# Kernel tuning notes

Measured on AMD Instinct MI355X. Metric: run time of the kernel, lower is better.

The kernel has to match this reference:

```python
import jax, jax.numpy as jnp
import numpy as np

D = 6
EPS = 1e-5


def layer_norm(x, w, b):
    m = jnp.mean(x, axis=-1, keepdims=True)
    v = jnp.mean(jnp.square(x - m), axis=-1, keepdims=True)
    return (x - m) * jax.lax.rsqrt(v + EPS) * w + b


def setup_inputs() -> dict:
    key = jax.random.key(0)
    ks = jax.random.split(key, 8)
    B, S = 8192, 128
    scale = 0.2
    return {
        "x": jax.random.normal(ks[0], (B, S, D), jnp.float32),
        "ln1_w": jnp.ones((D,), jnp.float32),
        "ln1_b": jnp.zeros((D,), jnp.float32),
        "wqkv": jax.random.normal(ks[1], (D, 3 * D), jnp.float32) * scale,
        "bqkv": jnp.zeros((3 * D,), jnp.float32),
        "wo": jax.random.normal(ks[2], (D, D), jnp.float32) * scale,
        "bo": jnp.zeros((D,), jnp.float32),
        "ln2_w": jnp.ones((D,), jnp.float32),
        "ln2_b": jnp.zeros((D,), jnp.float32),
        "w1": jax.random.normal(ks[3], (D, D), jnp.float32) * scale,
        "b1": jnp.zeros((D,), jnp.float32),
        "w2": jax.random.normal(ks[4], (D, D), jnp.float32) * scale,
        "b2": jnp.zeros((D,), jnp.float32),
    }


def reference(x, ln1_w, ln1_b, wqkv, bqkv, wo, bo, ln2_w, ln2_b, w1, b1, w2, b2):
    B, S, _ = x.shape
    # --- attention sub-block: x = x + attn(ln1(x)) ---
    h = layer_norm(x, ln1_w, ln1_b)                      # [B,S,D]
    qkv = h @ wqkv + bqkv                                # [B,S,3D]
    q, k, v = jnp.split(qkv, 3, axis=-1)
    scores = jnp.einsum('bqd,bkd->bqk', q, k) / jnp.sqrt(jnp.asarray(D, x.dtype))
    causal = jnp.tril(jnp.ones((S, S), bool))            # [S,S]
    scores = jnp.where(causal, scores, jnp.asarray(-1e9, x.dtype))
    attn = jax.nn.softmax(scores, axis=-1)               # [B,S,S]
    o = jnp.einsum('bqk,bkd->bqd', attn, v) @ wo + bo
    x = x + o
    # --- FFN sub-block: x = x + W2 @ gelu(W1 @ ln2(x)) ---
    h2 = layer_norm(x, ln2_w, ln2_b)
    ff = jax.nn.gelu(h2 @ w1 + b1, approximate=False) @ w2 + b2
    return x + ff
```

## Files before the change

### kernel.cpp

```cpp
#include <hip/hip_runtime.h>
#include <cmath>


typedef float v2f  __attribute__((ext_vector_type(2)));
typedef short s8v  __attribute__((ext_vector_type(8)));
typedef float f16v __attribute__((ext_vector_type(16)));

constexpr int D = 6;
constexpr int S = 128;
#define EPS 1e-5f
#define RSQRT_D 0.4082482904638631f
#define LOG2E   1.4426950408889634f

#define EXP2F(x) __builtin_amdgcn_exp2f(x)
#define RCPF(x)  __builtin_amdgcn_rcpf(x)

union U4 { uint32_t u[4]; s8v v; };

__device__ __forceinline__ uint32_t pkbf(float hi, float lo) {
    return __builtin_amdgcn_perm(__builtin_bit_cast(uint32_t, hi),
                                 __builtin_bit_cast(uint32_t, lo),
                                 0x07060302u);
}
__device__ __forceinline__ uint16_t bf16t(float x) {
    return (uint16_t)(__builtin_bit_cast(uint32_t, x) >> 16);
}

__global__ __launch_bounds__(S, 3) void txblock_kernel(
    const float* __restrict__ x,
    const float* __restrict__ ln1_w, const float* __restrict__ ln1_b,
    const float* __restrict__ wqkv,  const float* __restrict__ bqkv,
    const float* __restrict__ wo,    const float* __restrict__ bo,
    const float* __restrict__ ln2_w, const float* __restrict__ ln2_b,
    const float* __restrict__ w1,    const float* __restrict__ b1,
    const float* __restrict__ w2,    const float* __restrict__ b2,
    float* __restrict__ out)
{
    __shared__ uint32_t qlds[S][8];
    __shared__ uint32_t klds[S][8];
    __shared__ uint16_t vt[8][S];
    __shared__ float    obuf[S][8];

    const int b = blockIdx.x;
    const int s = threadIdx.x;
    const float* xrow = x + ((size_t)b * S + s) * D;
    float*      orow = out + ((size_t)b * S + s) * D;

    v2f xv01 = ((const v2f*)xrow)[0];
    v2f xv23 = ((const v2f*)xrow)[1];
    v2f xv45 = ((const v2f*)xrow)[2];
    float xv[D] = {xv01[0], xv01[1], xv23[0], xv23[1], xv45[0], xv45[1]};

    float m = 0.f;
    #pragma unroll
    for (int d = 0; d < D; ++d) m += xv[d];
    m *= (1.0f / D);
    float var = 0.f;
    #pragma unroll
    for (int d = 0; d < D; ++d) { float t = xv[d] - m; var += t * t; }
    var *= (1.0f / D);
    float rstd = rsqrtf(var + EPS);
    float h1[D];
    #pragma unroll
    for (int d = 0; d < D; ++d)
        h1[d] = (xv[d] - m) * rstd * ln1_w[d] + ln1_b[d];

    float q[D], kk[D], vv[D];
    #pragma unroll
    for (int j = 0; j < D; ++j) {
        float aq = bqkv[j], ak = bqkv[D + j], av = bqkv[2 * D + j];
        #pragma unroll
        for (int d = 0; d < D; ++d) {
            const float* wrow = wqkv + d * 3 * D;
            aq += h1[d] * wrow[j];
            ak += h1[d] * wrow[D + j];
            av += h1[d] * wrow[2 * D + j];
        }
        q[j]  = aq * (RSQRT_D * LOG2E);
        kk[j] = ak;
        vv[j] = av;
    }

    qlds[s][0] = pkbf(q[1], q[0]);
    qlds[s][1] = pkbf(q[3], q[2]);
    qlds[s][2] = pkbf(q[5], q[4]);
    qlds[s][3] = 0; qlds[s][4] = 0; qlds[s][5] = 0; qlds[s][6] = 0; qlds[s][7] = 0;
    klds[s][0] = pkbf(kk[1], kk[0]);
    klds[s][1] = pkbf(kk[3], kk[2]);
    klds[s][2] = pkbf(kk[5], kk[4]);
    klds[s][3] = 0; klds[s][4] = 0; klds[s][5] = 0; klds[s][6] = 0; klds[s][7] = 0;
    #pragma unroll
    for (int d = 0; d < D; ++d) vt[d][s] = bf16t(vv[d]);
    vt[6][s] = 0x3F80;
    vt[7][s] = 0;
    __syncthreads();

    const int wv = s >> 6;
    const int ln = s & 31;
    const int hw = (s >> 5) & 1;
    const int ne = (ln < 6) ? ln : 6;

    const int mt0 = wv ? 1 : 0;
    const int mt1 = wv ? 2 : 3;

    #pragma unroll
    for (int pass = 0; pass < 2; ++pass) {
        const int mt = pass ? mt1 : mt0;
        U4 qf; qf.v = *(const s8v*)&qlds[mt * 32 + ln][hw * 4];
        f16v O = (f16v)(0.0f);
        for (int kt = 0; kt <= mt; ++kt) {
            s8v kf = *(const s8v*)&klds[kt * 32 + ln][hw * 4];
            f16v c1 = __builtin_amdgcn_mfma_f32_32x32x16_bf16(
                          kf, qf.v, (f16v)(0.0f), 0, 0, 0);
            float p[16];
            #pragma unroll
            for (int r = 0; r < 16; ++r) p[r] = EXP2F(c1[r]);
            if (kt == mt) {
                #pragma unroll
                for (int r = 0; r < 16; ++r) {
                    int jl = (r & 3) + 8 * (r >> 2) + 4 * hw;
                    p[r] = (jl > ln) ? 0.0f : p[r];
                }
            }
            uint32_t pk[8], rp[8];
            #pragma unroll
            for (int t = 0; t < 8; ++t) pk[t] = pkbf(p[2 * t + 1], p[2 * t]);
            #pragma unroll
            for (int t = 0; t < 8; ++t)
                rp[t] = (uint32_t)__shfl_xor((int)pk[t], 32);
            U4 a1, a2;
            a1.u[0] = hw ? rp[2] : pk[0];
            a1.u[1] = hw ? rp[3] : pk[1];
            a1.u[2] = hw ? pk[2] : rp[0];
            a1.u[3] = hw ? pk[3] : rp[1];
            a2.u[0] = hw ? rp[6] : pk[4];
            a2.u[1] = hw ? rp[7] : pk[5];
            a2.u[2] = hw ? pk[6] : rp[4];
            a2.u[3] = hw ? pk[7] : rp[5];
            s8v b1 = *(const s8v*)&vt[ne][kt * 32 + hw * 8];
            s8v b2 = *(const s8v*)&vt[ne][kt * 32 + 16 + hw * 8];
            O = __builtin_amdgcn_mfma_f32_32x32x16_bf16(a1.v, b1, O, 0, 0, 0);
            O = __builtin_amdgcn_mfma_f32_32x32x16_bf16(a2.v, b2, O, 0, 0, 0);
        }
        if (ln < 7) {
            #pragma unroll
            for (int r = 0; r < 16; ++r) {
                int row = (r & 3) + 8 * (r >> 2) + 4 * hw;
                obuf[mt * 32 + row][ln] = O[r];
            }
        }
    }
    __syncthreads();

    float invl = RCPF(obuf[s][6]);
    float av6[D];
    #pragma unroll
    for (int d = 0; d < D; ++d) av6[d] = obuf[s][d] * invl;

    float x2[D];
    #pragma unroll
    for (int d = 0; d < D; ++d) {
        float o = bo[d];
        #pragma unroll
        for (int e = 0; e < D; ++e) o += av6[e] * wo[e * D + d];
        x2[d] = xv[d] + o;
    }

    float m2 = 0.f;
    #pragma unroll
    for (int d = 0; d < D; ++d) m2 += x2[d];
    m2 *= (1.0f / D);
    float var2 = 0.f;
    #pragma unroll
    for (int d = 0; d < D; ++d) { float t = x2[d] - m2; var2 += t * t; }
    var2 *= (1.0f / D);
    float rstd2 = rsqrtf(var2 + EPS);
    float h2[D];
    #pragma unroll
    for (int d = 0; d < D; ++d)
        h2[d] = (x2[d] - m2) * rstd2 * ln2_w[d] + ln2_b[d];

    float g[D];
    #pragma unroll
    for (int j = 0; j < D; ++j) {
        float a = b1[j];
        #pragma unroll
        for (int d = 0; d < D; ++d) a += h2[d] * w1[d * D + j];
        float t  = a * a;
        float in = fmaf(0.044715f * t, a, a);
        float e  = EXP2F(in * -2.3022229f);
        float r  = RCPF(1.0f + e);
        g[j] = a * r;
    }
    float og[D];
    #pragma unroll
    for (int d = 0; d < D; ++d) {
        float a = b2[d];
        #pragma unroll
        for (int e = 0; e < D; ++e) a += g[e] * w2[e * D + d];
        og[d] = x2[d] + a;
    }
    ((v2f*)orow)[0] = (v2f){og[0], og[1]};
    ((v2f*)orow)[1] = (v2f){og[2], og[3]};
    ((v2f*)orow)[2] = (v2f){og[4], og[5]};
}

extern "C" void kernel_launch(void* const* d_in, const int* in_sizes, int n_in,
                              void* d_out, int out_size, void* d_ws, size_t ws_size,
                              hipStream_t stream) {
    const float* x     = (const float*)d_in[0];
    const float* ln1_w = (const float*)d_in[1];
    const float* ln1_b = (const float*)d_in[2];
    const float* wqkv  = (const float*)d_in[3];
    const float* bqkv  = (const float*)d_in[4];
    const float* wo    = (const float*)d_in[5];
    const float* bo    = (const float*)d_in[6];
    const float* ln2_w = (const float*)d_in[7];
    const float* ln2_b = (const float*)d_in[8];
    const float* w1    = (const float*)d_in[9];
    const float* b1    = (const float*)d_in[10];
    const float* w2    = (const float*)d_in[11];
    const float* b2    = (const float*)d_in[12];
    float* out = (float*)d_out;

    const int B = in_sizes[0] / (S * D);
    txblock_kernel<<<B, S, 0, stream>>>(x, ln1_w, ln1_b, wqkv, bqkv, wo, bo,
                                        ln2_w, ln2_b, w1, b1, w2, b2, out);
}
```

Baseline: 122.3 us.

## Use packed FP32 FMAs, pad LDS arrays, fuse exp/mask/pack, raise occupancy

Result: faster. 118.6 us (-3.0%).

```diff
diff --git a/kernel.cpp b/kernel.cpp
--- a/kernel.cpp
+++ b/kernel.cpp
@@ -2,9 +2,10 @@
 #include <cmath>
 
 
-typedef float v2f  __attribute__((ext_vector_type(2)));
-typedef short s8v  __attribute__((ext_vector_type(8)));
-typedef float f16v __attribute__((ext_vector_type(16)));
+typedef float    v2f  __attribute__((ext_vector_type(2)));
+typedef uint32_t u2   __attribute__((ext_vector_type(2)));
+typedef short    s8v  __attribute__((ext_vector_type(8)));
+typedef float    f16v __attribute__((ext_vector_type(16)));
 
 constexpr int D = 6;
 constexpr int S = 128;
@@ -14,8 +15,9 @@
 
 #define EXP2F(x) __builtin_amdgcn_exp2f(x)
 #define RCPF(x)  __builtin_amdgcn_rcpf(x)
-
-union U4 { uint32_t u[4]; s8v v; };
+#define PKFMA(a, b, c) __builtin_elementwise_fma((a), (b), (c))
+
+union U4 { uint32_t u[4]; u2 h[2]; s8v v; };
 
 __device__ __forceinline__ uint32_t pkbf(float hi, float lo) {
     return __builtin_amdgcn_perm(__builtin_bit_cast(uint32_t, hi),
@@ -26,7 +28,7 @@
     return (uint16_t)(__builtin_bit_cast(uint32_t, x) >> 16);
 }
 
-__global__ __launch_bounds__(S, 3) void txblock_kernel(
+__global__ __launch_bounds__(S, 4) void txblock_kernel(
     const float* __restrict__ x,
     const float* __restrict__ ln1_w, const float* __restrict__ ln1_b,
     const float* __restrict__ wqkv,  const float* __restrict__ bqkv,
@@ -36,10 +38,10 @@
     const float* __restrict__ w2,    const float* __restrict__ b2,
     float* __restrict__ out)
 {
-    __shared__ uint32_t qlds[S][8];
-    __shared__ uint32_t klds[S][8];
-    __shared__ uint16_t vt[8][S];
-    __shared__ float    obuf[S][8];
+    __shared__ uint32_t qlds[S][10];
+    __shared__ uint32_t klds[S][10];
+    __shared__ uint16_t vt[8][S + 8];
+    __shared__ float    obuf[S][10];
 
     const int b = blockIdx.x;
     const int s = threadIdx.x;
@@ -65,32 +67,40 @@
     for (int d = 0; d < D; ++d)
         h1[d] = (xv[d] - m) * rstd * ln1_w[d] + ln1_b[d];
 
-    float q[D], kk[D], vv[D];
-    #pragma unroll
-    for (int j = 0; j < D; ++j) {
-        float aq = bqkv[j], ak = bqkv[D + j], av = bqkv[2 * D + j];
-        #pragma unroll
-        for (int d = 0; d < D; ++d) {
-            const float* wrow = wqkv + d * 3 * D;
-            aq += h1[d] * wrow[j];
-            ak += h1[d] * wrow[D + j];
-            av += h1[d] * wrow[2 * D + j];
-        }
-        q[j]  = aq * (RSQRT_D * LOG2E);
-        kk[j] = ak;
-        vv[j] = av;
-    }
-
-    qlds[s][0] = pkbf(q[1], q[0]);
-    qlds[s][1] = pkbf(q[3], q[2]);
-    qlds[s][2] = pkbf(q[5], q[4]);
-    qlds[s][3] = 0; qlds[s][4] = 0; qlds[s][5] = 0; qlds[s][6] = 0; qlds[s][7] = 0;
-    klds[s][0] = pkbf(kk[1], kk[0]);
-    klds[s][1] = pkbf(kk[3], kk[2]);
-    klds[s][2] = pkbf(kk[5], kk[4]);
-    klds[s][3] = 0; klds[s][4] = 0; klds[s][5] = 0; klds[s][6] = 0; klds[s][7] = 0;
-    #pragma unroll
-    for (int d = 0; d < D; ++d) vt[d][s] = bf16t(vv[d]);
+    v2f aq[3], ak[3], av[3];
+    #pragma unroll
+    for (int jp = 0; jp < 3; ++jp) {
+        aq[jp] = ((const v2f*)bqkv)[jp];
+        ak[jp] = ((const v2f*)(bqkv + D))[jp];
+        av[jp] = ((const v2f*)(bqkv + 2 * D))[jp];
+    }
+    #pragma unroll
+    for (int d = 0; d < D; ++d) {
+        const float* wrow = wqkv + d * 3 * D;
+        v2f hd = {h1[d], h1[d]};
+        #pragma unroll
+        for (int jp = 0; jp < 3; ++jp) {
+            aq[jp] = PKFMA(hd, ((const v2f*)wrow)[jp], aq[jp]);
+            ak[jp] = PKFMA(hd, ((const v2f*)(wrow + D))[jp], ak[jp]);
+            av[jp] = PKFMA(hd, ((const v2f*)(wrow + 2 * D))[jp], av[jp]);
+        }
+    }
+    const v2f qscale = {RSQRT_D * LOG2E, RSQRT_D * LOG2E};
+
+    #pragma unroll
+    for (int jp = 0; jp < 3; ++jp) {
+        v2f qs = aq[jp] * qscale;
+        qlds[s][jp] = pkbf(qs[1], qs[0]);
+        klds[s][jp] = pkbf(ak[jp][1], ak[jp][0]);
+    }
+    #pragma unroll
+    for (int c = 3; c < 8; ++c) { qlds[s][c] = 0; klds[s][c] = 0; }
+    vt[0][s] = bf16t(av[0][0]);
+    vt[1][s] = bf16t(av[0][1]);
+    vt[2][s] = bf16t(av[1][0]);
+    vt[3][s] = bf16t(av[1][1]);
+    vt[4][s] = bf16t(av[2][0]);
+    vt[5][s] = bf16t(av[2][1]);
     vt[6][s] = 0x3F80;
     vt[7][s] = 0;
     __syncthreads();
@@ -106,28 +116,34 @@
     #pragma unroll
     for (int pass = 0; pass < 2; ++pass) {
         const int mt = pass ? mt1 : mt0;
-        U4 qf; qf.v = *(const s8v*)&qlds[mt * 32 + ln][hw * 4];
+        U4 qf;
+        {
+            const u2* p = (const u2*)&qlds[mt * 32 + ln][hw * 4];
+            qf.h[0] = p[0]; qf.h[1] = p[1];
+        }
         f16v O = (f16v)(0.0f);
         for (int kt = 0; kt <= mt; ++kt) {
-            s8v kf = *(const s8v*)&klds[kt * 32 + ln][hw * 4];
+            U4 kf;
+            {
+                const u2* p = (const u2*)&klds[kt * 32 + ln][hw * 4];
+                kf.h[0] = p[0]; kf.h[1] = p[1];
+            }
             f16v c1 = __builtin_amdgcn_mfma_f32_32x32x16_bf16(
-                          kf, qf.v, (f16v)(0.0f), 0, 0, 0);
-            float p[16];
-            #pragma unroll
-            for (int r = 0; r < 16; ++r) p[r] = EXP2F(c1[r]);
-            if (kt == mt) {
-                #pragma unroll
-                for (int r = 0; r < 16; ++r) {
-                    int jl = (r & 3) + 8 * (r >> 2) + 4 * hw;
-                    p[r] = (jl > ln) ? 0.0f : p[r];
-                }
-            }
+                          kf.v, qf.v, (f16v)(0.0f), 0, 0, 0);
             uint32_t pk[8], rp[8];
             #pragma unroll
-            for (int t = 0; t < 8; ++t) pk[t] = pkbf(p[2 * t + 1], p[2 * t]);
-            #pragma unroll
-            for (int t = 0; t < 8; ++t)
+            for (int t = 0; t < 8; ++t) {
+                float p0 = EXP2F(c1[2 * t]);
+                float p1 = EXP2F(c1[2 * t + 1]);
+                if (kt == mt) {
+                    const int j0 = ((2 * t) & 3) + 8 * ((2 * t) >> 2) + 4 * hw;
+                    const int j1 = ((2 * t + 1) & 3) + 8 * ((2 * t + 1) >> 2) + 4 * hw;
+                    p0 = (j0 > ln) ? 0.0f : p0;
+                    p1 = (j1 > ln) ? 0.0f : p1;
+                }
+                pk[t] = pkbf(p1, p0);
                 rp[t] = (uint32_t)__shfl_xor((int)pk[t], 32);
+            }
             U4 a1, a2;
             a1.u[0] = hw ? rp[2] : pk[0];
             a1.u[1] = hw ? rp[3] : pk[1];
@@ -137,10 +153,10 @@
             a2.u[1] = hw ? rp[7] : pk[5];
             a2.u[2] = hw ? pk[6] : rp[4];
             a2.u[3] = hw ? pk[7] : rp[5];
-            s8v b1 = *(const s8v*)&vt[ne][kt * 32 + hw * 8];
-            s8v b2 = *(const s8v*)&vt[ne][kt * 32 + 16 + hw * 8];
-            O = __builtin_amdgcn_mfma_f32_32x32x16_bf16(a1.v, b1, O, 0, 0, 0);
-            O = __builtin_amdgcn_mfma_f32_32x32x16_bf16(a2.v, b2, O, 0, 0, 0);
+            s8v vb1 = *(const s8v*)&vt[ne][kt * 32 + hw * 8];
+            s8v vb2 = *(const s8v*)&vt[ne][kt * 32 + 16 + hw * 8];
+            O = __builtin_amdgcn_mfma_f32_32x32x16_bf16(a1.v, vb1, O, 0, 0, 0);
+            O = __builtin_amdgcn_mfma_f32_32x32x16_bf16(a2.v, vb2, O, 0, 0, 0);
         }
         if (ln < 7) {
             #pragma unroll
@@ -152,19 +168,28 @@
     }
     __syncthreads();
 
+    v2f o01 = *(const v2f*)&obuf[s][0];
+    v2f o23 = *(const v2f*)&obuf[s][2];
+    v2f o45 = *(const v2f*)&obuf[s][4];
     float invl = RCPF(obuf[s][6]);
-    float av6[D];
-    #pragma unroll
-    for (int d = 0; d < D; ++d) av6[d] = obuf[s][d] * invl;
-
-    float x2[D];
-    #pragma unroll
-    for (int d = 0; d < D; ++d) {
-        float o = bo[d];
-        #pragma unroll
-        for (int e = 0; e < D; ++e) o += av6[e] * wo[e * D + d];
-        x2[d] = xv[d] + o;
-    }
+    v2f il = {invl, invl};
+    o01 *= il; o23 *= il; o45 *= il;
+    float av6[D] = {o01[0], o01[1], o23[0], o23[1], o45[0], o45[1]};
+
+    v2f xvp[3] = {xv01, xv23, xv45};
+    v2f x2p[3];
+    #pragma unroll
+    for (int dp = 0; dp < 3; ++dp) {
+        v2f o = ((const v2f*)bo)[dp];
+        #pragma unroll
+        for (int e = 0; e < D; ++e) {
+            v2f we = ((const v2f*)(wo + e * D))[dp];
+            v2f ae = {av6[e], av6[e]};
+            o = PKFMA(ae, we, o);
+        }
+        x2p[dp] = o + xvp[dp];
+    }
+    float x2[D] = {x2p[0][0], x2p[0][1], x2p[1][0], x2p[1][1], x2p[2][0], x2p[2][1]};
 
     float m2 = 0.f;
     #pragma unroll
@@ -180,29 +205,39 @@
     for (int d = 0; d < D; ++d)
         h2[d] = (x2[d] - m2) * rstd2 * ln2_w[d] + ln2_b[d];
 
+    v2f ap[3];
+    #pragma unroll
+    for (int jp = 0; jp < 3; ++jp) {
+        v2f a = ((const v2f*)b1)[jp];
+        #pragma unroll
+        for (int d = 0; d < D; ++d) {
+            v2f wd = ((const v2f*)(w1 + d * D))[jp];
+            v2f hd = {h2[d], h2[d]};
+            a = PKFMA(hd, wd, a);
+        }
+        ap[jp] = a;
+    }
     float g[D];
     #pragma unroll
     for (int j = 0; j < D; ++j) {
-        float a = b1[j];
-        #pragma unroll
-        for (int d = 0; d < D; ++d) a += h2[d] * w1[d * D + j];
+        float a = ap[j >> 1][j & 1];
         float t  = a * a;
         float in = fmaf(0.044715f * t, a, a);
         float e  = EXP2F(in * -2.3022229f);
         float r  = RCPF(1.0f + e);
         g[j] = a * r;
     }
-    float og[D];
-    #pragma unroll
-    for (int d = 0; d < D; ++d) {
-        float a = b2[d];
-        #pragma unroll
-        for (int e = 0; e < D; ++e) a += g[e] * w2[e * D + d];
-        og[d] = x2[d] + a;
-    }
-    ((v2f*)orow)[0] = (v2f){og[0], og[1]};
-    ((v2f*)orow)[1] = (v2f){og[2], og[3]};
-    ((v2f*)orow)[2] = (v2f){og[4], og[5]};
+    #pragma unroll
+    for (int dp = 0; dp < 3; ++dp) {
+        v2f a = ((const v2f*)b2)[dp];
+        #pragma unroll
+        for (int e = 0; e < D; ++e) {
+            v2f we = ((const v2f*)(w2 + e * D))[dp];
+            v2f ge = {g[e], g[e]};
+            a = PKFMA(ge, we, a);
+        }
+        ((v2f*)orow)[dp] = x2p[dp] + a;
+    }
 }
 
 extern "C" void kernel_launch(void* const* d_in, const int* in_sizes, int n_in,
```
